# Kernel tuning notes

Measured on AMD Instinct MI355X. Metric: run time of the kernel, lower is better.

The kernel has to match this reference:

```python
import jax, jax.numpy as jnp
import numpy as np

N_NODES = 100000
N_EDGES = 1600000
F_IN, HIDDEN, N_CLASS = 64, 48, 40


def setup_inputs() -> dict:
    key = jax.random.key(0)
    ks = jax.random.split(key, 9)
    def glorot(k, fi, fo):
        s = (6.0 / (fi + fo)) ** 0.5
        return jax.random.uniform(k, (fi, fo), jnp.float32, -s, s)
    return {
        "x": jax.random.normal(ks[0], (N_NODES, F_IN), jnp.float32),
        "edge_index": jax.random.randint(ks[1], (2, N_EDGES), 0, N_NODES, jnp.int64),
        "edge_weight": jax.random.uniform(ks[2], (N_EDGES,), jnp.float32),
        "W1": glorot(ks[3], F_IN, HIDDEN),   # ARMAConv init_weight (K=1)
        "V1": glorot(ks[4], F_IN, HIDDEN),   # ARMAConv root_weight
        "b1": jnp.zeros((HIDDEN,), jnp.float32),
        "W2": glorot(ks[5], HIDDEN, N_CLASS),
        "V2": glorot(ks[6], HIDDEN, N_CLASS),
        "b2": jnp.zeros((N_CLASS,), jnp.float32),
    }


def _arma_conv(x, W, V, b, src, dst, norm, num_nodes):
    # out = ReLU( A_norm @ (x @ W) + x @ V + b )   (num_stacks=1, num_layers=1)
    h = x @ W                                   # [N, F_out]
    msg = h[src] * norm[:, None]                # gather + scale  [E, F_out]
    agg = jax.ops.segment_sum(msg, dst, num_segments=num_nodes)  # scatter-add
    return jax.nn.relu(agg + x @ V + b)


def reference(x, edge_index, edge_weight, W1, V1, b1, W2, V2, b2):
    num_nodes = x.shape[0]
    src, dst = edge_index[0], edge_index[1]
    # gcn_norm, add_self_loops=False: D^{-1/2} A D^{-1/2}
    deg = jax.ops.segment_sum(edge_weight, dst, num_segments=num_nodes)
    dinv = jnp.where(deg > 0, jax.lax.rsqrt(jnp.where(deg > 0, deg, 1.0)), 0.0)
    norm = dinv[src] * edge_weight * dinv[dst]
    # eval mode: input dropout is identity
    h = _arma_conv(x, W1, V1, b1, src, dst, norm, num_nodes)
    h = _arma_conv(h, W2, V2, b2, src, dst, norm, num_nodes)
    return jax.nn.log_softmax(h, axis=-1)
```

## Files before the change

### kernel.cpp

```cpp
#include <hip/hip_runtime.h>
#include <math.h>


constexpr int F_IN = 64;
constexpr int HIDDEN = 48;
constexpr int N_CLASS = 40;
constexpr int CHUNK = 8192;
constexpr int BIN_SHIFT = 9;
constexpr int CSR_CAP = 12288;

typedef __attribute__((ext_vector_type(8))) short bf16x8;
typedef __attribute__((ext_vector_type(4))) float f32x4;

__device__ __forceinline__ short bfr(float f) {
    unsigned u = __float_as_uint(f);
    return (short)((u + 0x7fffu + ((u >> 16) & 1u)) >> 16);
}
__device__ __forceinline__ unsigned pack_bf2(float a, float b) {
    unsigned ua = __float_as_uint(a), ub = __float_as_uint(b);
    ua = (ua + 0x7fffu + ((ua >> 16) & 1u)) >> 16;
    ub = (ub + 0x7fffu + ((ub >> 16) & 1u)) >> 16;
    return ua | (ub << 16);
}
__device__ __forceinline__ float2 unpack_bf2(unsigned u) {
    return make_float2(__uint_as_float(u << 16), __uint_as_float(u & 0xffff0000u));
}
__device__ __forceinline__ bf16x8 cvt8(float4 f0, float4 f1) {
    bf16x8 r;
    r[0] = bfr(f0.x); r[1] = bfr(f0.y); r[2] = bfr(f0.z); r[3] = bfr(f0.w);
    r[4] = bfr(f1.x); r[5] = bfr(f1.y); r[6] = bfr(f1.z); r[7] = bfr(f1.w);
    return r;
}

__device__ __forceinline__ void mfma_gemm1_body(char* smem, const float* __restrict__ X,
                                                const float* __restrict__ W,
                                                const float* __restrict__ V,
                                                const float* __restrict__ b,
                                                unsigned* __restrict__ XWp,
                                                unsigned* __restrict__ AGGp, int N,
                                                int gb, int tid) {
    short* sWT = (short*)smem;
    float* ep = (float*)(smem + 12288);
    for (int i = tid; i < 96 * 64; i += 256) {
        int c = i >> 6, k = i & 63;
        float v = (c < 48) ? W[k * 48 + c] : V[k * 48 + (c - 48)];
        sWT[i] = bfr(v);
    }
    __syncthreads();

    int lane = tid & 63, wv = tid >> 6;
    int m = lane & 15, quad = lane >> 4;
    int nb0 = gb * 64;
    int n = nb0 + wv * 16 + m;

    bf16x8 a0, a1;
    if (n < N) {
        const float4* xr = (const float4*)(X + (size_t)n * 64 + quad * 8);
        a0 = cvt8(xr[0], xr[1]);
        const float4* xr2 = (const float4*)(X + (size_t)n * 64 + 32 + quad * 8);
        a1 = cvt8(xr2[0], xr2[1]);
    } else {
        for (int j = 0; j < 8; ++j) { a0[j] = 0; a1[j] = 0; }
    }

    f32x4 acc[6];
#pragma unroll
    for (int ct = 0; ct < 6; ++ct) acc[ct] = (f32x4){0.f, 0.f, 0.f, 0.f};
#pragma unroll
    for (int ct = 0; ct < 6; ++ct) {
        bf16x8 b0 = *(const bf16x8*)(sWT + (ct * 16 + m) * 64 + quad * 8);
        bf16x8 b1 = *(const bf16x8*)(sWT + (ct * 16 + m) * 64 + 32 + quad * 8);
        acc[ct] = __builtin_amdgcn_mfma_f32_16x16x32_bf16(a0, b0, acc[ct], 0, 0, 0);
        acc[ct] = __builtin_amdgcn_mfma_f32_16x16x32_bf16(a1, b1, acc[ct], 0, 0, 0);
    }
#pragma unroll
    for (int ct = 0; ct < 6; ++ct)
#pragma unroll
        for (int r = 0; r < 4; ++r)
            ep[(wv * 16 + quad * 4 + r) * 96 + ct * 16 + m] = acc[ct][r];
    __syncthreads();
    for (int i = tid; i < 64 * 24; i += 256) {
        int r = i / 24, c2 = i - r * 24;
        int node = nb0 + r;
        if (node >= N) continue;
        float w0 = ep[r * 96 + 2 * c2], w1 = ep[r * 96 + 2 * c2 + 1];
        XWp[node * 24 + c2] = pack_bf2(w0, w1);
        float v0 = ep[r * 96 + 48 + 2 * c2], v1 = ep[r * 96 + 48 + 2 * c2 + 1];
        float2 bb = ((const float2*)b)[c2];
        AGGp[node * 24 + c2] = pack_bf2(v0 + bb.x, v1 + bb.y);
    }
}

__global__ __launch_bounds__(256) void count_gemm1(
    const int* __restrict__ dst, int* __restrict__ binCnt, int E, int nCountBlocks,
    const float* __restrict__ X, const float* __restrict__ W,
    const float* __restrict__ V, const float* __restrict__ b,
    unsigned* __restrict__ XWp, unsigned* __restrict__ AGGp, int N) {
    __shared__ char smem[36864];
    if ((int)blockIdx.x < nCountBlocks) {
        int* hist = (int*)smem;
        int tid = threadIdx.x;
        hist[tid] = 0;
        __syncthreads();
        long long e0 = (long long)blockIdx.x * CHUNK;
        int M = (int)min((long long)CHUNK, (long long)E - e0);
        for (int i = tid; i < M; i += 256) atomicAdd(&hist[dst[e0 + i] >> BIN_SHIFT], 1);
        __syncthreads();
        atomicAdd(&binCnt[tid], hist[tid]);
    } else {
        mfma_gemm1_body(smem, X, W, V, b, XWp, AGGp, N,
                        (int)blockIdx.x - nCountBlocks, (int)threadIdx.x);
    }
}

__global__ void scan_bins(const int* __restrict__ binCnt, int* __restrict__ binStart,
                          int* __restrict__ binCursor, int* __restrict__ rowPtr,
                          int E, int N) {
    __shared__ int s[256];
    int t = threadIdx.x;
    int v = binCnt[t];
    s[t] = v;
    __syncthreads();
#pragma unroll
    for (int o = 1; o < 256; o <<= 1) {
        int u = (t >= o) ? s[t - o] : 0;
        __syncthreads();
        s[t] += u;
        __syncthreads();
    }
    int excl = s[t] - v;
    binStart[t] = excl;
    binCursor[t] = excl;
    if (t == 0) {
        binStart[256] = E;
        rowPtr[N] = E;
    }
}

__global__ void binscatter(const int* __restrict__ src, const int* __restrict__ dst,
                           const float* __restrict__ w, int* __restrict__ binCursor,
                           int2* __restrict__ binned, int E) {
    __shared__ int sx[CHUNK];
    __shared__ int sw[CHUNK];
    __shared__ unsigned char sbin[CHUNK];
    __shared__ int hist[256];
    int tid = threadIdx.x;
    hist[tid] = 0;
    __syncthreads();
    long long e0 = (long long)blockIdx.x * CHUNK;
    int M = (int)min((long long)CHUNK, (long long)E - e0);
    for (int i = tid; i < M; i += 256) {
        int d = dst[e0 + i];
        int bn = d >> BIN_SHIFT;
        sx[i] = ((d & 511) << 17) | src[e0 + i];
        sw[i] = __float_as_int(w[e0 + i]);
        sbin[i] = (unsigned char)bn;
        atomicAdd(&hist[bn], 1);
    }
    __syncthreads();
    int base = atomicAdd(&binCursor[tid], hist[tid]);
    __syncthreads();
    hist[tid] = base;
    __syncthreads();
    for (int i = tid; i < M; i += 256) {
        int p = atomicAdd(&hist[sbin[i]], 1);
        binned[p] = make_int2(sx[i], sw[i]);
    }
}

__global__ __launch_bounds__(512) void build_csr(const int2* __restrict__ binned,
                                                 const int* __restrict__ binStart,
                                                 int* __restrict__ rowPtr,
                                                 float* __restrict__ dinv,
                                                 unsigned* __restrict__ csr, int N) {
    __shared__ int sx[CSR_CAP];
    __shared__ int sw[CSR_CAP];
    __shared__ int cntL[512];
    __shared__ float degL[512];
    __shared__ int scanL[512];
    int b = blockIdx.x, tid = threadIdx.x;
    int e0 = binStart[b], e1 = binStart[b + 1], M = e1 - e0;
    cntL[tid] = 0;
    degL[tid] = 0.f;
    __syncthreads();
    bool fits = (M <= CSR_CAP);
    for (int i = tid; i < M; i += 512) {
        int2 p = binned[e0 + i];
        if (fits) { sx[i] = p.x; sw[i] = p.y; }
        int dl = ((unsigned)p.x) >> 17;
        atomicAdd(&cntL[dl], 1);
        atomicAdd(&degL[dl], __int_as_float(p.y));
    }
    __syncthreads();
    int v = cntL[tid];
    scanL[tid] = v;
    __syncthreads();
#pragma unroll
    for (int o = 1; o < 512; o <<= 1) {
        int u = (tid >= o) ? scanL[tid - o] : 0;
        __syncthreads();
        scanL[tid] += u;
        __syncthreads();
    }
    int excl = scanL[tid] - v;
    int node = (b << BIN_SHIFT) + tid;
    float dg = degL[tid];
    float dv = dg > 0.f ? rsqrtf(dg) : 0.f;
    if (node < N) {
        rowPtr[node] = e0 + excl;
        dinv[node] = dv;
    }
    cntL[tid] = e0 + excl;
    degL[tid] = dv;
    __syncthreads();
    for (int i = tid; i < M; i += 512) {
        int px, pw;
        if (fits) { px = sx[i]; pw = sw[i]; }
        else { int2 p = binned[e0 + i]; px = p.x; pw = p.y; }
        int dl = ((unsigned)px) >> 17;
        int pos = atomicAdd(&cntL[dl], 1);
        float wn = __int_as_float(pw) * degL[dl];
        unsigned uw = __float_as_uint(wn);
        uw = (uw + 0x7fffu + ((uw >> 16) & 1u)) >> 16;
        csr[pos] = ((unsigned)(px & 0x1FFFF) << 15) | uw;
    }
}

__global__ void scale_xw(unsigned* __restrict__ XWp, const float* __restrict__ dinv,
                         int total) {
    int t = blockIdx.x * blockDim.x + threadIdx.x;
    if (t >= total) return;
    float dv = dinv[t / 24];
    float2 u = unpack_bf2(XWp[t]);
    XWp[t] = pack_bf2(u.x * dv, u.y * dv);
}

template <int W>
__device__ __forceinline__ float4 row_accum2(const unsigned* __restrict__ XWp,
                                             const unsigned* __restrict__ csr,
                                             int j, int end, int c, float4 s) {
    while (j < end && (j & 3)) {
        unsigned p = csr[j++];
        uint2 u = *(const uint2*)(XWp + (p >> 15) * W + c);
        float nr = __uint_as_float((p & 0x7FFFu) << 16);
        float2 x0 = unpack_bf2(u.x), x1 = unpack_bf2(u.y);
        s.x = fmaf(x0.x, nr, s.x); s.y = fmaf(x0.y, nr, s.y);
        s.z = fmaf(x1.x, nr, s.z); s.w = fmaf(x1.y, nr, s.w);
    }
    for (; j + 4 <= end; j += 4) {
        uint4 p4 = *(const uint4*)(csr + j);
        uint2 u0 = *(const uint2*)(XWp + (p4.x >> 15) * W + c);
        uint2 u1 = *(const uint2*)(XWp + (p4.y >> 15) * W + c);
        uint2 u2 = *(const uint2*)(XWp + (p4.z >> 15) * W + c);
        uint2 u3 = *(const uint2*)(XWp + (p4.w >> 15) * W + c);
        float n0 = __uint_as_float((p4.x & 0x7FFFu) << 16);
        float n1 = __uint_as_float((p4.y & 0x7FFFu) << 16);
        float n2 = __uint_as_float((p4.z & 0x7FFFu) << 16);
        float n3 = __uint_as_float((p4.w & 0x7FFFu) << 16);
        float2 a0 = unpack_bf2(u0.x), b0 = unpack_bf2(u0.y);
        float2 a1 = unpack_bf2(u1.x), b1 = unpack_bf2(u1.y);
        float2 a2 = unpack_bf2(u2.x), b2 = unpack_bf2(u2.y);
        float2 a3 = unpack_bf2(u3.x), b3 = unpack_bf2(u3.y);
        s.x = fmaf(a0.x, n0, s.x); s.y = fmaf(a0.y, n0, s.y);
        s.z = fmaf(b0.x, n0, s.z); s.w = fmaf(b0.y, n0, s.w);
        s.x = fmaf(a1.x, n1, s.x); s.y = fmaf(a1.y, n1, s.y);
        s.z = fmaf(b1.x, n1, s.z); s.w = fmaf(b1.y, n1, s.w);
        s.x = fmaf(a2.x, n2, s.x); s.y = fmaf(a2.y, n2, s.y);
        s.z = fmaf(b2.x, n2, s.z); s.w = fmaf(b2.y, n2, s.w);
        s.x = fmaf(a3.x, n3, s.x); s.y = fmaf(a3.y, n3, s.y);
        s.z = fmaf(b3.x, n3, s.z); s.w = fmaf(b3.y, n3, s.w);
    }
    for (; j < end; ++j) {
        unsigned p = csr[j];
        uint2 u = *(const uint2*)(XWp + (p >> 15) * W + c);
        float nr = __uint_as_float((p & 0x7FFFu) << 16);
        float2 x0 = unpack_bf2(u.x), x1 = unpack_bf2(u.y);
        s.x = fmaf(x0.x, nr, s.x); s.y = fmaf(x0.y, nr, s.y);
        s.z = fmaf(x1.x, nr, s.z); s.w = fmaf(x1.y, nr, s.w);
    }
    return s;
}

__global__ __launch_bounds__(384) void pull_agg(const unsigned* __restrict__ XWp,
                                                const unsigned* __restrict__ csr,
                                                const int* __restrict__ rowPtr,
                                                const unsigned* __restrict__ AGG1p,
                                                unsigned* __restrict__ H1p, int N) {
    int t = blockIdx.x * blockDim.x + threadIdx.x;
    int n = t / 12, c1 = t - n * 12;
    if (n >= N) return;
    int c = 2 * c1;
    uint2 a = *(const uint2*)(AGG1p + n * 24 + c);
    float2 f0 = unpack_bf2(a.x), f1 = unpack_bf2(a.y);
    float4 s = make_float4(f0.x, f0.y, f1.x, f1.y);
    s = row_accum2<24>(XWp, csr, rowPtr[n], rowPtr[n + 1], c, s);
    uint2 o;
    o.x = pack_bf2(fmaxf(s.x, 0.f), fmaxf(s.y, 0.f));
    o.y = pack_bf2(fmaxf(s.z, 0.f), fmaxf(s.w, 0.f));
    *(uint2*)(H1p + n * 24 + c) = o;
}

__global__ __launch_bounds__(256) void gemm2_kernel(
    const short* __restrict__ H1, const float* __restrict__ W,
    const float* __restrict__ V, const float* __restrict__ b,
    const float* __restrict__ dinv, unsigned* __restrict__ XWp,
    unsigned* __restrict__ AGGp, int N) {
    __shared__ char smem[30720];
    short* sWT = (short*)smem;
    float* ep = (float*)(smem + 10240);
    int tid = threadIdx.x;
    for (int i = tid; i < 80 * 64; i += 256) {
        int c = i >> 6, k = i & 63;
        float v = 0.f;
        if (k < 48) v = (c < 40) ? W[k * 40 + c] : V[k * 40 + (c - 40)];
        sWT[i] = bfr(v);
    }
    __syncthreads();

    int lane = tid & 63, wv = tid >> 6;
    int m = lane & 15, quad = lane >> 4;
    int nb0 = (int)blockIdx.x * 64;
    int n = nb0 + wv * 16 + m;

    bf16x8 a0, a1;
    if (n < N) {
        a0 = *(const bf16x8*)(H1 + (size_t)n * 48 + quad * 8);
        if (quad < 2) {
            a1 = *(const bf16x8*)(H1 + (size_t)n * 48 + 32 + quad * 8);
        } else {
            for (int j = 0; j < 8; ++j) a1[j] = 0;
        }
    } else {
        for (int j = 0; j < 8; ++j) { a0[j] = 0; a1[j] = 0; }
    }

    f32x4 acc[5];
#pragma unroll
    for (int ct = 0; ct < 5; ++ct) acc[ct] = (f32x4){0.f, 0.f, 0.f, 0.f};
#pragma unroll
    for (int ct = 0; ct < 5; ++ct) {
        bf16x8 b0 = *(const bf16x8*)(sWT + (ct * 16 + m) * 64 + quad * 8);
        bf16x8 b1 = *(const bf16x8*)(sWT + (ct * 16 + m) * 64 + 32 + quad * 8);
        acc[ct] = __builtin_amdgcn_mfma_f32_16x16x32_bf16(a0, b0, acc[ct], 0, 0, 0);
        acc[ct] = __builtin_amdgcn_mfma_f32_16x16x32_bf16(a1, b1, acc[ct], 0, 0, 0);
    }
#pragma unroll
    for (int ct = 0; ct < 5; ++ct)
#pragma unroll
        for (int r = 0; r < 4; ++r)
            ep[(wv * 16 + quad * 4 + r) * 80 + ct * 16 + m] = acc[ct][r];
    __syncthreads();
    for (int i = tid; i < 64 * 20; i += 256) {
        int r = i / 20, c2 = i - r * 20;
        int node = nb0 + r;
        if (node >= N) continue;
        float dv = dinv[node];
        float w0 = ep[r * 80 + 2 * c2], w1 = ep[r * 80 + 2 * c2 + 1];
        XWp[node * 20 + c2] = pack_bf2(w0 * dv, w1 * dv);
        float v0 = ep[r * 80 + 40 + 2 * c2], v1 = ep[r * 80 + 40 + 2 * c2 + 1];
        float2 bb = ((const float2*)b)[c2];
        AGGp[node * 20 + c2] = pack_bf2(v0 + bb.x, v1 + bb.y);
    }
}

__global__ __launch_bounds__(320) void pull_ls(const unsigned* __restrict__ XWp,
                                               const unsigned* __restrict__ csr,
                                               const int* __restrict__ rowPtr,
                                               const unsigned* __restrict__ AGG2p,
                                               float* __restrict__ out, int N) {
    __shared__ float4 sbuf[32 * 10];
    __shared__ float sl[32];
    int tid = threadIdx.x;
    int nl = tid / 10, c1 = tid - nl * 10;
    int n = blockIdx.x * 32 + nl;
    int c = 2 * c1;
    float4 s = make_float4(0.f, 0.f, 0.f, 0.f);
    if (n < N) {
        uint2 a = *(const uint2*)(AGG2p + n * 20 + c);
        float2 f0 = unpack_bf2(a.x), f1 = unpack_bf2(a.y);
        s = make_float4(f0.x, f0.y, f1.x, f1.y);
        s = row_accum2<20>(XWp, csr, rowPtr[n], rowPtr[n + 1], c, s);
    }
    sbuf[nl * 10 + c1] = s;
    __syncthreads();
    if (tid < 32) {
        float m = 0.f;
        for (int k = 0; k < 10; ++k) {
            float4 v = sbuf[tid * 10 + k];
            m = fmaxf(m, fmaxf(fmaxf(v.x, v.y), fmaxf(v.z, v.w)));
        }
        float sum = 0.f;
        for (int k = 0; k < 10; ++k) {
            float4 v = sbuf[tid * 10 + k];
            sum += expf(fmaxf(v.x, 0.f) - m) + expf(fmaxf(v.y, 0.f) - m) +
                   expf(fmaxf(v.z, 0.f) - m) + expf(fmaxf(v.w, 0.f) - m);
        }
        sl[tid] = m + logf(sum);
    }
    __syncthreads();
    if (n < N) {
        float l = sl[nl];
        ((float4*)out)[n * 10 + c1] =
            make_float4(fmaxf(s.x, 0.f) - l, fmaxf(s.y, 0.f) - l,
                        fmaxf(s.z, 0.f) - l, fmaxf(s.w, 0.f) - l);
    }
}

extern "C" void kernel_launch(void* const* d_in, const int* in_sizes, int n_in,
                              void* d_out, int out_size, void* d_ws, size_t ws_size,
                              hipStream_t stream) {
    const float* x  = (const float*)d_in[0];
    const int*   ei = (const int*)d_in[1];
    const float* ew = (const float*)d_in[2];
    const float* W1 = (const float*)d_in[3];
    const float* V1 = (const float*)d_in[4];
    const float* b1 = (const float*)d_in[5];
    const float* W2 = (const float*)d_in[6];
    const float* V2 = (const float*)d_in[7];
    const float* b2 = (const float*)d_in[8];
    float* out = (float*)d_out;

    const int N = in_sizes[0] / F_IN;
    const int E = in_sizes[2];
    const int* src = ei;
    const int* dst = ei + E;

    char* ws = (char*)d_ws;
    size_t off = 0;
    auto carve = [&](size_t bytes) {
        void* p = ws + off;
        off = (off + bytes + 255) & ~size_t(255);
        return p;
    };
    int*      binCnt    = (int*)carve(256 * 4);
    int*      binStart  = (int*)carve(257 * 4);
    int*      binCursor = (int*)carve(256 * 4);
    int*      rowPtr    = (int*)carve((size_t)(N + 1) * 4);
    float*    dinv      = (float*)carve((size_t)N * 4);
    int2*     binned    = (int2*)carve((size_t)E * 8);
    unsigned* csr       = (unsigned*)carve((size_t)E * 4);
    unsigned* xW1p      = (unsigned*)carve((size_t)N * 24 * 4);
    unsigned* agg1p     = (unsigned*)carve((size_t)N * 24 * 4);
    unsigned* h1p       = (unsigned*)carve((size_t)N * 24 * 4);
    unsigned* xW2p      = (unsigned*)carve((size_t)N * 20 * 4);
    unsigned* agg2p     = (unsigned*)carve((size_t)N * 20 * 4);

    const int B = 256;
    auto cdiv = [](long long a, long long b) { return (int)((a + b - 1) / b); };
    const int nChunks = cdiv(E, CHUNK);
    const int nBins = (N + (1 << BIN_SHIFT) - 1) >> BIN_SHIFT;
    const int nGemmBlocks = cdiv(N, 64);

    hipMemsetAsync(binCnt, 0, 256 * 4, stream);

    count_gemm1<<<nChunks + nGemmBlocks, B, 0, stream>>>(dst, binCnt, E, nChunks,
                                                         x, W1, V1, b1, xW1p, agg1p, N);
    scan_bins<<<1, 256, 0, stream>>>(binCnt, binStart, binCursor, rowPtr, E, N);
    binscatter<<<nChunks, B, 0, stream>>>(src, dst, ew, binCursor, binned, E);
    build_csr<<<nBins, 512, 0, stream>>>(binned, binStart, rowPtr, dinv, csr, N);

    scale_xw<<<cdiv((long long)N * 24, B), B, 0, stream>>>(xW1p, dinv, N * 24);

    pull_agg<<<cdiv((long long)N * 12, 384), 384, 0, stream>>>(xW1p, csr, rowPtr,
                                                               agg1p, h1p, N);

    gemm2_kernel<<<nGemmBlocks, B, 0, stream>>>((const short*)h1p, W2, V2, b2,
                                                dinv, xW2p, agg2p, N);

    pull_ls<<<cdiv(N, 32), 320, 0, stream>>>(xW2p, csr, rowPtr, agg2p, out, N);
}
```

Measured before the change: 278.3 us.

## Fuse xW scaling into CSR build, shrink scatter chunks, unroll gathers by eight

The separate scale_xw launch is removed and its work is folded into the end of build_csr, which already holds dinv for its bin of nodes. build_csr also drops its LDS staging of the binned edges and rereads them from global memory, which frees shared memory and raises occupancy. binscatter now uses smaller chunks, so more blocks share the work. The CSR gather loop is unrolled to eight edges, and streaming loads use nontemporal hints to avoid polluting the cache. The costs are a second global read of the binned array, more atomic contention on binCursor, and higher register pressure in the pull kernels.

```diff
diff --git a/kernel.cpp b/kernel.cpp
--- a/kernel.cpp
+++ b/kernel.cpp
@@ -5,12 +5,14 @@
 constexpr int F_IN = 64;
 constexpr int HIDDEN = 48;
 constexpr int N_CLASS = 40;
-constexpr int CHUNK = 8192;
+constexpr int CHUNK_CNT = 8192;
+constexpr int CHUNK_SC = 2048;
 constexpr int BIN_SHIFT = 9;
-constexpr int CSR_CAP = 12288;
 
 typedef __attribute__((ext_vector_type(8))) short bf16x8;
 typedef __attribute__((ext_vector_type(4))) float f32x4;
+typedef __attribute__((ext_vector_type(4))) unsigned u32x4;
+typedef __attribute__((ext_vector_type(2))) unsigned u32x2;
 
 __device__ __forceinline__ short bfr(float f) {
     unsigned u = __float_as_uint(f);
@@ -102,9 +104,10 @@
         int tid = threadIdx.x;
         hist[tid] = 0;
         __syncthreads();
-        long long e0 = (long long)blockIdx.x * CHUNK;
-        int M = (int)min((long long)CHUNK, (long long)E - e0);
-        for (int i = tid; i < M; i += 256) atomicAdd(&hist[dst[e0 + i] >> BIN_SHIFT], 1);
+        long long e0 = (long long)blockIdx.x * CHUNK_CNT;
+        int M = (int)min((long long)CHUNK_CNT, (long long)E - e0);
+        for (int i = tid; i < M; i += 256)
+            atomicAdd(&hist[__builtin_nontemporal_load(&dst[e0 + i]) >> BIN_SHIFT], 1);
         __syncthreads();
         atomicAdd(&binCnt[tid], hist[tid]);
     } else {
@@ -137,23 +140,24 @@
     }
 }
 
-__global__ void binscatter(const int* __restrict__ src, const int* __restrict__ dst,
-                           const float* __restrict__ w, int* __restrict__ binCursor,
-                           int2* __restrict__ binned, int E) {
-    __shared__ int sx[CHUNK];
-    __shared__ int sw[CHUNK];
-    __shared__ unsigned char sbin[CHUNK];
+__global__ __launch_bounds__(256) void binscatter(
+    const int* __restrict__ src, const int* __restrict__ dst,
+    const float* __restrict__ w, int* __restrict__ binCursor,
+    int2* __restrict__ binned, int E) {
+    __shared__ int sx[CHUNK_SC];
+    __shared__ int sw[CHUNK_SC];
+    __shared__ unsigned char sbin[CHUNK_SC];
     __shared__ int hist[256];
     int tid = threadIdx.x;
     hist[tid] = 0;
     __syncthreads();
-    long long e0 = (long long)blockIdx.x * CHUNK;
-    int M = (int)min((long long)CHUNK, (long long)E - e0);
+    long long e0 = (long long)blockIdx.x * CHUNK_SC;
+    int M = (int)min((long long)CHUNK_SC, (long long)E - e0);
     for (int i = tid; i < M; i += 256) {
-        int d = dst[e0 + i];
+        int d = __builtin_nontemporal_load(&dst[e0 + i]);
         int bn = d >> BIN_SHIFT;
-        sx[i] = ((d & 511) << 17) | src[e0 + i];
-        sw[i] = __float_as_int(w[e0 + i]);
+        sx[i] = ((d & 511) << 17) | __builtin_nontemporal_load(&src[e0 + i]);
+        sw[i] = __float_as_int(__builtin_nontemporal_load(&w[e0 + i]));
         sbin[i] = (unsigned char)bn;
         atomicAdd(&hist[bn], 1);
     }
@@ -172,9 +176,8 @@
                                                  const int* __restrict__ binStart,
                                                  int* __restrict__ rowPtr,
                                                  float* __restrict__ dinv,
-                                                 unsigned* __restrict__ csr, int N) {
-    __shared__ int sx[CSR_CAP];
-    __shared__ int sw[CSR_CAP];
+                                                 unsigned* __restrict__ csr,
+                                                 unsigned* __restrict__ XW1p, int N) {
     __shared__ int cntL[512];
     __shared__ float degL[512];
     __shared__ int scanL[512];
@@ -183,10 +186,8 @@
     cntL[tid] = 0;
     degL[tid] = 0.f;
     __syncthreads();
-    bool fits = (M <= CSR_CAP);
     for (int i = tid; i < M; i += 512) {
         int2 p = binned[e0 + i];
-        if (fits) { sx[i] = p.x; sw[i] = p.y; }
         int dl = ((unsigned)p.x) >> 17;
         atomicAdd(&cntL[dl], 1);
         atomicAdd(&degL[dl], __int_as_float(p.y));
@@ -214,25 +215,23 @@
     degL[tid] = dv;
     __syncthreads();
     for (int i = tid; i < M; i += 512) {
-        int px, pw;
-        if (fits) { px = sx[i]; pw = sw[i]; }
-        else { int2 p = binned[e0 + i]; px = p.x; pw = p.y; }
-        int dl = ((unsigned)px) >> 17;
+        int2 p = binned[e0 + i];
+        int dl = ((unsigned)p.x) >> 17;
         int pos = atomicAdd(&cntL[dl], 1);
-        float wn = __int_as_float(pw) * degL[dl];
+        float wn = __int_as_float(p.y) * degL[dl];
         unsigned uw = __float_as_uint(wn);
         uw = (uw + 0x7fffu + ((uw >> 16) & 1u)) >> 16;
-        csr[pos] = ((unsigned)(px & 0x1FFFF) << 15) | uw;
-    }
-}
-
-__global__ void scale_xw(unsigned* __restrict__ XWp, const float* __restrict__ dinv,
-                         int total) {
-    int t = blockIdx.x * blockDim.x + threadIdx.x;
-    if (t >= total) return;
-    float dv = dinv[t / 24];
-    float2 u = unpack_bf2(XWp[t]);
-    XWp[t] = pack_bf2(u.x * dv, u.y * dv);
+        csr[pos] = ((unsigned)(p.x & 0x1FFFF) << 15) | uw;
+    }
+    int nb0 = b << BIN_SHIFT;
+    for (int i = tid; i < 512 * 24; i += 512) {
+        int nl = i / 24, c = i - nl * 24;
+        int nn = nb0 + nl;
+        if (nn >= N) break;
+        float dvn = degL[nl];
+        float2 u = unpack_bf2(XW1p[nn * 24 + c]);
+        XW1p[nn * 24 + c] = pack_bf2(u.x * dvn, u.y * dvn);
+    }
 }
 
 template <int W>
@@ -241,18 +240,63 @@
                                              int j, int end, int c, float4 s) {
     while (j < end && (j & 3)) {
         unsigned p = csr[j++];
-        uint2 u = *(const uint2*)(XWp + (p >> 15) * W + c);
+        u32x2 u = *(const u32x2*)(XWp + (p >> 15) * W + c);
         float nr = __uint_as_float((p & 0x7FFFu) << 16);
         float2 x0 = unpack_bf2(u.x), x1 = unpack_bf2(u.y);
         s.x = fmaf(x0.x, nr, s.x); s.y = fmaf(x0.y, nr, s.y);
         s.z = fmaf(x1.x, nr, s.z); s.w = fmaf(x1.y, nr, s.w);
     }
-    for (; j + 4 <= end; j += 4) {
-        uint4 p4 = *(const uint4*)(csr + j);
-        uint2 u0 = *(const uint2*)(XWp + (p4.x >> 15) * W + c);
-        uint2 u1 = *(const uint2*)(XWp + (p4.y >> 15) * W + c);
-        uint2 u2 = *(const uint2*)(XWp + (p4.z >> 15) * W + c);
-        uint2 u3 = *(const uint2*)(XWp + (p4.w >> 15) * W + c);
+    for (; j + 8 <= end; j += 8) {
+        u32x4 pa = __builtin_nontemporal_load((const u32x4*)(csr + j));
+        u32x4 pb = __builtin_nontemporal_load((const u32x4*)(csr + j + 4));
+        u32x2 u0 = *(const u32x2*)(XWp + (pa.x >> 15) * W + c);
+        u32x2 u1 = *(const u32x2*)(XWp + (pa.y >> 15) * W + c);
+        u32x2 u2 = *(const u32x2*)(XWp + (pa.z >> 15) * W + c);
+        u32x2 u3 = *(const u32x2*)(XWp + (pa.w >> 15) * W + c);
+        u32x2 u4 = *(const u32x2*)(XWp + (pb.x >> 15) * W + c);
+        u32x2 u5 = *(const u32x2*)(XWp + (pb.y >> 15) * W + c);
+        u32x2 u6 = *(const u32x2*)(XWp + (pb.z >> 15) * W + c);
+        u32x2 u7 = *(const u32x2*)(XWp + (pb.w >> 15) * W + c);
+        float n0 = __uint_as_float((pa.x & 0x7FFFu) << 16);
+        float n1 = __uint_as_float((pa.y & 0x7FFFu) << 16);
+        float n2 = __uint_as_float((pa.z & 0x7FFFu) << 16);
+        float n3 = __uint_as_float((pa.w & 0x7FFFu) << 16);
+        float n4 = __uint_as_float((pb.x & 0x7FFFu) << 16);
+        float n5 = __uint_as_float((pb.y & 0x7FFFu) << 16);
+        float n6 = __uint_as_float((pb.z & 0x7FFFu) << 16);
+        float n7 = __uint_as_float((pb.w & 0x7FFFu) << 16);
+        float2 a0 = unpack_bf2(u0.x), b0 = unpack_bf2(u0.y);
+        float2 a1 = unpack_bf2(u1.x), b1 = unpack_bf2(u1.y);
+        float2 a2 = unpack_bf2(u2.x), b2 = unpack_bf2(u2.y);
+        float2 a3 = unpack_bf2(u3.x), b3 = unpack_bf2(u3.y);
+        float2 a4 = unpack_bf2(u4.x), b4 = unpack_bf2(u4.y);
+        float2 a5 = unpack_bf2(u5.x), b5 = unpack_bf2(u5.y);
+        float2 a6 = unpack_bf2(u6.x), b6 = unpack_bf2(u6.y);
+        float2 a7 = unpack_bf2(u7.x), b7 = unpack_bf2(u7.y);
+        s.x = fmaf(a0.x, n0, s.x); s.y = fmaf(a0.y, n0, s.y);
+        s.z = fmaf(b0.x, n0, s.z); s.w = fmaf(b0.y, n0, s.w);
+        s.x = fmaf(a1.x, n1, s.x); s.y = fmaf(a1.y, n1, s.y);
+        s.z = fmaf(b1.x, n1, s.z); s.w = fmaf(b1.y, n1, s.w);
+        s.x = fmaf(a2.x, n2, s.x); s.y = fmaf(a2.y, n2, s.y);
+        s.z = fmaf(b2.x, n2, s.z); s.w = fmaf(b2.y, n2, s.w);
+        s.x = fmaf(a3.x, n3, s.x); s.y = fmaf(a3.y, n3, s.y);
+        s.z = fmaf(b3.x, n3, s.z); s.w = fmaf(b3.y, n3, s.w);
+        s.x = fmaf(a4.x, n4, s.x); s.y = fmaf(a4.y, n4, s.y);
+        s.z = fmaf(b4.x, n4, s.z); s.w = fmaf(b4.y, n4, s.w);
+        s.x = fmaf(a5.x, n5, s.x); s.y = fmaf(a5.y, n5, s.y);
+        s.z = fmaf(b5.x, n5, s.z); s.w = fmaf(b5.y, n5, s.w);
+        s.x = fmaf(a6.x, n6, s.x); s.y = fmaf(a6.y, n6, s.y);
+        s.z = fmaf(b6.x, n6, s.z); s.w = fmaf(b6.y, n6, s.w);
+        s.x = fmaf(a7.x, n7, s.x); s.y = fmaf(a7.y, n7, s.y);
+        s.z = fmaf(b7.x, n7, s.z); s.w = fmaf(b7.y, n7, s.w);
+    }
+    if (j + 4 <= end) {
+        u32x4 p4 = __builtin_nontemporal_load((const u32x4*)(csr + j));
+        j += 4;
+        u32x2 u0 = *(const u32x2*)(XWp + (p4.x >> 15) * W + c);
+        u32x2 u1 = *(const u32x2*)(XWp + (p4.y >> 15) * W + c);
+        u32x2 u2 = *(const u32x2*)(XWp + (p4.z >> 15) * W + c);
+        u32x2 u3 = *(const u32x2*)(XWp + (p4.w >> 15) * W + c);
         float n0 = __uint_as_float((p4.x & 0x7FFFu) << 16);
         float n1 = __uint_as_float((p4.y & 0x7FFFu) << 16);
         float n2 = __uint_as_float((p4.z & 0x7FFFu) << 16);
@@ -272,7 +316,7 @@
     }
     for (; j < end; ++j) {
         unsigned p = csr[j];
-        uint2 u = *(const uint2*)(XWp + (p >> 15) * W + c);
+        u32x2 u = *(const u32x2*)(XWp + (p >> 15) * W + c);
         float nr = __uint_as_float((p & 0x7FFFu) << 16);
         float2 x0 = unpack_bf2(u.x), x1 = unpack_bf2(u.y);
         s.x = fmaf(x0.x, nr, s.x); s.y = fmaf(x0.y, nr, s.y);
@@ -290,14 +334,14 @@
     int n = t / 12, c1 = t - n * 12;
     if (n >= N) return;
     int c = 2 * c1;
-    uint2 a = *(const uint2*)(AGG1p + n * 24 + c);
+    u32x2 a = __builtin_nontemporal_load((const u32x2*)(AGG1p + n * 24 + c));
     float2 f0 = unpack_bf2(a.x), f1 = unpack_bf2(a.y);
     float4 s = make_float4(f0.x, f0.y, f1.x, f1.y);
     s = row_accum2<24>(XWp, csr, rowPtr[n], rowPtr[n + 1], c, s);
-    uint2 o;
+    u32x2 o;
     o.x = pack_bf2(fmaxf(s.x, 0.f), fmaxf(s.y, 0.f));
     o.y = pack_bf2(fmaxf(s.z, 0.f), fmaxf(s.w, 0.f));
-    *(uint2*)(H1p + n * 24 + c) = o;
+    *(u32x2*)(H1p + n * 24 + c) = o;
 }
 
 __global__ __launch_bounds__(256) void gemm2_kernel(
@@ -376,7 +420,7 @@
     int c = 2 * c1;
     float4 s = make_float4(0.f, 0.f, 0.f, 0.f);
     if (n < N) {
-        uint2 a = *(const uint2*)(AGG2p + n * 20 + c);
+        u32x2 a = __builtin_nontemporal_load((const u32x2*)(AGG2p + n * 20 + c));
         float2 f0 = unpack_bf2(a.x), f1 = unpack_bf2(a.y);
         s = make_float4(f0.x, f0.y, f1.x, f1.y);
         s = row_accum2<20>(XWp, csr, rowPtr[n], rowPtr[n + 1], c, s);
@@ -447,19 +491,18 @@
 
     const int B = 256;
     auto cdiv = [](long long a, long long b) { return (int)((a + b - 1) / b); };
-    const int nChunks = cdiv(E, CHUNK);
+    const int nCnt = cdiv(E, CHUNK_CNT);
+    const int nSc = cdiv(E, CHUNK_SC);
     const int nBins = (N + (1 << BIN_SHIFT) - 1) >> BIN_SHIFT;
     const int nGemmBlocks = cdiv(N, 64);
 
     hipMemsetAsync(binCnt, 0, 256 * 4, stream);
 
-    count_gemm1<<<nChunks + nGemmBlocks, B, 0, stream>>>(dst, binCnt, E, nChunks,
-                                                         x, W1, V1, b1, xW1p, agg1p, N);
+    count_gemm1<<<nCnt + nGemmBlocks, B, 0, stream>>>(dst, binCnt, E, nCnt,
+                                                      x, W1, V1, b1, xW1p, agg1p, N);
     scan_bins<<<1, 256, 0, stream>>>(binCnt, binStart, binCursor, rowPtr, E, N);
-    binscatter<<<nChunks, B, 0, stream>>>(src, dst, ew, binCursor, binned, E);
-    build_csr<<<nBins, 512, 0, stream>>>(binned, binStart, rowPtr, dinv, csr, N);
-
-    scale_xw<<<cdiv((long long)N * 24, B), B, 0, stream>>>(xW1p, dinv, N * 24);
+    binscatter<<<nSc, B, 0, stream>>>(src, dst, ew, binCursor, binned, E);
+    build_csr<<<nBins, 512, 0, stream>>>(binned, binStart, rowPtr, dinv, csr, xW1p, N);
 
     pull_agg<<<cdiv((long long)N * 12, 384), 384, 0, stream>>>(xW1p, csr, rowPtr,
                                                                agg1p, h1p, N);
```

After: 288.1 us. 1.04x slower.
